# Kernel tuning notes

Hardware: AMD Instinct MI355X
Metric: run time of the kernel (lower is better)

Reference implementation:

```python
import jax, jax.numpy as jnp
import numpy as np

B, M, D, E, K = 4096, 4, 1024, 8, 2
H = 4 * D  # expert hidden dim (input_dim * 4)


def setup_inputs() -> dict:
    key = jax.random.key(0)
    k0, k1, k2, k3 = jax.random.split(key, 4)
    x = jax.random.normal(k0, (B, M, D), jnp.float32)
    Wg = jax.random.normal(k1, (D, E), jnp.float32) * (D ** -0.5)
    bg = jnp.zeros((E,), jnp.float32)
    W1 = jax.random.normal(k2, (E, D, H), jnp.float32) * (D ** -0.5)
    b1 = jnp.zeros((E, H), jnp.float32)
    W2 = jax.random.normal(k3, (E, H, D), jnp.float32) * (H ** -0.5)
    b2 = jnp.zeros((E, D), jnp.float32)
    return {"x": x, "Wg": Wg, "bg": bg, "W1": W1, "b1": b1, "W2": W2, "b2": b2}


def reference(x, Wg, bg, W1, b1, W2, b2):
    Bn, Mn, Dn = x.shape
    xf = x.reshape(-1, Dn)                      # [N, D], N = B*M
    logits = xf @ Wg + bg                       # [N, E] gating scores (eval: no noise)
    topv, topi = jax.lax.top_k(logits, K)       # [N, K]
    topw = jax.nn.softmax(topv, axis=-1)        # softmax over top-k only
    # scatter top-k weights into dense [N, E] gate matrix (zeros elsewhere)
    gates = jnp.sum(jax.nn.one_hot(topi, E, dtype=xf.dtype) * topw[..., None], axis=1)

    def body(acc, p):
        W1e, b1e, W2e, b2e, ge = p
        # Expert MLP: Linear -> exact GELU (torch nn.GELU default) -> Linear
        y = jax.nn.gelu(xf @ W1e + b1e, approximate=False) @ W2e + b2e
        return acc + ge[:, None] * y, None

    out, _ = jax.lax.scan(body, jnp.zeros_like(xf), (W1, b1, W2, b2, gates.T))
    return out.reshape(Bn, Mn, Dn)
```

## Files before the change

kernel.cpp:

```cpp
#include <hip/hip_runtime.h>
#include <hip/hip_bf16.h>
#include <cstdint>
#include <cstddef>

#define NTOK 16384
#define DIM 1024
#define NEXP 8
#define HDIM 4096
#define BM 256
#define BN 256
#define BK 64
#define MAXTILES 160
#define GRIDX_COMB 160
#define GRIDX_FALL 80
#define GEMM_SMEM 131072

typedef unsigned short u16;
typedef short bf16x8 __attribute__((ext_vector_type(8)));
typedef float f32x4 __attribute__((ext_vector_type(4)));

typedef const __attribute__((address_space(1))) void* gas_ptr;
typedef __attribute__((address_space(3))) void* las_ptr;

__device__ __forceinline__ void gload16(const void* g, void* l) {
  __builtin_amdgcn_global_load_lds((gas_ptr)g, (las_ptr)l, 16, 0, 0);
}

__device__ __forceinline__ u16 f2b(float f) {
  union { float f; unsigned u; } v;
  v.f = f;
  unsigned r = v.u + 0x7fffu + ((v.u >> 16) & 1u);
  return (u16)(r >> 16);
}

__device__ __forceinline__ int2 swz_block() {
  int GX = gridDim.x;
  int nwg = GX * (int)gridDim.y;
  int bid = (int)blockIdx.y * GX + (int)blockIdx.x;
  int q = nwg >> 3, r = nwg & 7;
  int xcd = bid & 7, idx = bid >> 3;
  int wg = (xcd < r) ? (xcd * (q + 1) + idx)
                     : (r * (q + 1) + (xcd - r) * q + idx);
  return make_int2(wg % GX, wg / GX);
}

__global__ __launch_bounds__(256) void gating_kernel(
    const float* __restrict__ x, const float* __restrict__ Wg,
    const float* __restrict__ bg, int* __restrict__ e01,
    float2* __restrict__ w01, int* __restrict__ counts, u16* __restrict__ xb)
{
  __shared__ float4 wgl[NEXP][256];
  __shared__ int lcnt[16];
  int t = threadIdx.x;
  if (t < 16) lcnt[t] = 0;
  float* wglf = (float*)wgl;
  const float4* wg4 = (const float4*)Wg;
  for (int i = t; i < 2048; i += 256) {
    float4 v = wg4[i];
    int d = i >> 1, eb = (i & 1) * 4;
    wglf[(eb + 0) * 1024 + d] = v.x;
    wglf[(eb + 1) * 1024 + d] = v.y;
    wglf[(eb + 2) * 1024 + d] = v.z;
    wglf[(eb + 3) * 1024 + d] = v.w;
  }
  __syncthreads();
  int lane = t & 63, wid = t >> 6;
  int tok0 = blockIdx.x * 16 + wid * 4;
  for (int s = 0; s < 4; ++s) {
    int n = tok0 + s;
    const float4* xr = (const float4*)(x + (size_t)n * DIM);
    float4 xv[4];
    #pragma unroll
    for (int k = 0; k < 4; ++k) xv[k] = xr[lane + k * 64];
    ushort4* xo = (ushort4*)(xb + (size_t)n * DIM);
    #pragma unroll
    for (int k = 0; k < 4; ++k) {
      ushort4 o;
      o.x = f2b(xv[k].x); o.y = f2b(xv[k].y); o.z = f2b(xv[k].z); o.w = f2b(xv[k].w);
      xo[lane + k * 64] = o;
    }
    double acc[NEXP];
    #pragma unroll
    for (int e = 0; e < NEXP; ++e) acc[e] = 0.0;
    #pragma unroll
    for (int k = 0; k < 4; ++k) {
      #pragma unroll
      for (int e = 0; e < NEXP; ++e) {
        float4 w = wgl[e][lane + k * 64];
        acc[e] += (double)(xv[k].x * w.x) + (double)(xv[k].y * w.y)
                + (double)(xv[k].z * w.z) + (double)(xv[k].w * w.w);
      }
    }
    #pragma unroll
    for (int e = 0; e < NEXP; ++e) {
      for (int off = 32; off; off >>= 1) acc[e] += __shfl_down(acc[e], off, 64);
    }
    if (lane == 0) {
      float v[NEXP];
      #pragma unroll
      for (int e = 0; e < NEXP; ++e) v[e] = (float)acc[e] + bg[e];
      int e0 = 0; float v0 = v[0];
      #pragma unroll
      for (int e = 1; e < NEXP; ++e) if (v[e] > v0) { v0 = v[e]; e0 = e; }
      int e1 = -1; float v1 = -1e30f;
      #pragma unroll
      for (int e = 0; e < NEXP; ++e) if (e != e0 && v[e] > v1) { v1 = v[e]; e1 = e; }
      float d = expf(v1 - v0);
      float w0 = 1.0f / (1.0f + d);
      float w1 = d * w0;
      e01[n] = e0 | (e1 << 8);
      w01[n] = make_float2(w0, w1);
      atomicAdd(&lcnt[e0], 1);
      atomicAdd(&lcnt[8 + e1], 1);
    }
  }
  __syncthreads();
  if (t < 16 && lcnt[t]) atomicAdd(&counts[t], lcnt[t]);
}

__global__ void plan_kernel(const int* __restrict__ counts, int* __restrict__ offsets,
                            int* __restrict__ cursors, int* __restrict__ numTiles,
                            int4* __restrict__ tiledir, int combined)
{
  if (threadIdx.x == 0 && blockIdx.x == 0) {
    for (int p = 0; p < 2; ++p) {
      int o = 0;
      for (int e = 0; e < NEXP; ++e) {
        offsets[p * 8 + e] = o;
        cursors[p * 8 + e] = o;
        o += counts[p * 8 + e];
      }
    }
    if (combined) {
      int idx = 0;
      for (int s = 0; s < 16; ++s) {
        int p = s >> 3, e = s & 7;
        int c = counts[s];
        int base = p * NTOK + offsets[s];
        for (int st = 0; st < c; st += BM) {
          tiledir[idx] = make_int4(e, base + st, (c - st) < BM ? (c - st) : BM, 0);
          ++idx;
        }
      }
      numTiles[0] = idx;
      numTiles[1] = 0;
    } else {
      for (int p = 0; p < 2; ++p) {
        int idx = 0;
        for (int e = 0; e < NEXP; ++e) {
          int c = counts[p * 8 + e];
          int base = p * NTOK + offsets[p * 8 + e];
          for (int st = 0; st < c; st += BM) {
            tiledir[p * MAXTILES + idx] = make_int4(e, base + st, (c - st) < BM ? (c - st) : BM, 0);
            ++idx;
          }
        }
        numTiles[p] = idx;
      }
    }
  }
}

__global__ __launch_bounds__(256) void scatter_kernel(
    const int* __restrict__ e01, const float2* __restrict__ w01,
    int* __restrict__ cursors, int* __restrict__ rowlist, float* __restrict__ roww)
{
  int n = blockIdx.x * 256 + threadIdx.x;
  int ee = e01[n];
  float2 w = w01[n];
  int e0 = ee & 255, e1 = ee >> 8;
  int p0 = atomicAdd(&cursors[e0], 1);
  rowlist[p0] = n; roww[p0] = w.x;
  int p1 = atomicAdd(&cursors[8 + e1], 1);
  rowlist[NTOK + p1] = n; roww[NTOK + p1] = w.y;
}

__global__ __launch_bounds__(256) void transpose_convert_kernel(
    const float* __restrict__ in, u16* __restrict__ out, int R, int C)
{
  __shared__ float tile[64][65];
  size_t base = (size_t)blockIdx.z * R * C;
  int r0 = blockIdx.x * 64, c0 = blockIdx.y * 64;
  int t = threadIdx.x;
  int lr = t >> 4, lc4 = (t & 15) * 4;
  #pragma unroll
  for (int i = 0; i < 4; ++i) {
    float4 v = *reinterpret_cast<const float4*>(
        &in[base + (size_t)(r0 + i * 16 + lr) * C + c0 + lc4]);
    tile[i * 16 + lr][lc4 + 0] = v.x;
    tile[i * 16 + lr][lc4 + 1] = v.y;
    tile[i * 16 + lr][lc4 + 2] = v.z;
    tile[i * 16 + lr][lc4 + 3] = v.w;
  }
  __syncthreads();
  #pragma unroll
  for (int i = 0; i < 4; ++i) {
    int oc = i * 16 + lr;
    ushort4 o;
    o.x = f2b(tile[lc4 + 0][oc]);
    o.y = f2b(tile[lc4 + 1][oc]);
    o.z = f2b(tile[lc4 + 2][oc]);
    o.w = f2b(tile[lc4 + 3][oc]);
    *reinterpret_cast<ushort4*>(&out[base + (size_t)(c0 + oc) * R + r0 + lc4]) = o;
  }
}


__global__ __launch_bounds__(512, 2) void gemm1_kernel(
    const u16* __restrict__ xb, const u16* __restrict__ w1t,
    const float* __restrict__ b1, u16* __restrict__ h,
    const int* __restrict__ rowlist, const int4* __restrict__ tiledir,
    const int* __restrict__ numTiles, int hbase)
{
  extern __shared__ u16 smem[];
  u16* Aldsb = smem;
  u16* Bldsb = smem + 32768;
  __shared__ int tok[BM];
  int2 bxy = swz_block();
  int bx = bxy.x, by = bxy.y;
  if (bx >= *numTiles) return;
  int4 td = tiledir[bx];
  int e = td.x, row0 = td.y, rows = td.z;
  int n0 = by * BN;
  int t = threadIdx.x, lane = t & 63, wid = t >> 6;
  for (int i = t; i < BM; i += 512) {
    int p = row0 + i; if (p > 2 * NTOK - 1) p = 2 * NTOK - 1;
    tok[i] = rowlist[p];
  }
  __syncthreads();
  int schunk = (lane & 7) ^ (lane >> 3);
  const u16* gA[4]; const u16* gB[4];
  #pragma unroll
  for (int i = 0; i < 4; ++i) {
    int row = (wid * 4 + i) * 8 + (lane >> 3);
    gA[i] = xb + (size_t)tok[row] * DIM + schunk * 8;
    gB[i] = w1t + ((size_t)e * HDIM + n0 + row) * DIM + schunk * 8;
  }
  f32x4 acc[8][4] = {};
  int wr = wid >> 2, wc = wid & 3;
  int arow = lane & 15, cbase = lane >> 4, csw = arow & 7;
  #pragma unroll
  for (int i = 0; i < 4; ++i) {
    gload16(gA[i], &Aldsb[(wid * 4 + i) * 512]);
    gload16(gB[i], &Bldsb[(wid * 4 + i) * 512]);
  }
  __syncthreads();
  const int NKT = DIM / BK;
  for (int kt = 0; kt < NKT; ++kt) {
    int buf = kt & 1;
    if (kt + 1 < NKT) {
      int bo = (buf ^ 1) * 16384;
      #pragma unroll
      for (int i = 0; i < 4; ++i) {
        gload16(gA[i] + (kt + 1) * BK, &Aldsb[bo + (wid * 4 + i) * 512]);
        gload16(gB[i] + (kt + 1) * BK, &Bldsb[bo + (wid * 4 + i) * 512]);
      }
    }
    const u16* Ab = Aldsb + buf * 16384;
    const u16* Bb = Bldsb + buf * 16384;
    #pragma unroll
    for (int kk = 0; kk < 2; ++kk) {
      int cp = ((kk * 4 + cbase) ^ csw) * 8;
      bf16x8 a[8], b[4];
      #pragma unroll
      for (int m = 0; m < 8; ++m)
        a[m] = *reinterpret_cast<const bf16x8*>(&Ab[(wr * 128 + m * 16 + arow) * BK + cp]);
      #pragma unroll
      for (int n = 0; n < 4; ++n)
        b[n] = *reinterpret_cast<const bf16x8*>(&Bb[(wc * 64 + n * 16 + arow) * BK + cp]);
      __builtin_amdgcn_s_setprio(1);
      #pragma unroll
      for (int m = 0; m < 8; ++m)
        #pragma unroll
        for (int n = 0; n < 4; ++n)
          acc[m][n] = __builtin_amdgcn_mfma_f32_16x16x32_bf16(a[m], b[n], acc[m][n], 0, 0, 0);
      __builtin_amdgcn_s_setprio(0);
    }
    __syncthreads();
  }
  int rsub = (lane >> 4) * 4;
  #pragma unroll
  for (int m = 0; m < 8; ++m) {
    int lrb = wr * 128 + m * 16 + rsub;
    #pragma unroll
    for (int n = 0; n < 4; ++n) {
      int col = n0 + wc * 64 + n * 16 + arow;
      float bv = b1[e * HDIM + col];
      #pragma unroll
      for (int r = 0; r < 4; ++r) {
        int lr = lrb + r;
        if (lr < rows) {
          float v = acc[m][n][r] + bv;
          v = 0.5f * v * (1.0f + erff(v * 0.70710678118654752f));
          h[(size_t)(row0 + lr - hbase) * HDIM + col] = f2b(v);
        }
      }
    }
  }
}

__global__ __launch_bounds__(512, 2) void gemm2_kernel(
    const u16* __restrict__ h, const u16* __restrict__ w2t,
    const float* __restrict__ b2, float* __restrict__ out,
    const int* __restrict__ rowlist, const float* __restrict__ roww,
    const int4* __restrict__ tiledir, const int* __restrict__ numTiles, int hbase)
{
  extern __shared__ u16 smem[];
  u16* Aldsb = smem;
  u16* Bldsb = smem + 32768;
  __shared__ int tok[BM];
  __shared__ float wt[BM];
  int2 bxy = swz_block();
  int bx = bxy.x, by = bxy.y;
  if (bx >= *numTiles) return;
  int4 td = tiledir[bx];
  int e = td.x, row0 = td.y, rows = td.z;
  int n0 = by * BN;
  int t = threadIdx.x, lane = t & 63, wid = t >> 6;
  for (int i = t; i < BM; i += 512) {
    int p = row0 + i; if (p > 2 * NTOK - 1) p = 2 * NTOK - 1;
    tok[i] = rowlist[p];
    wt[i] = roww[p];
  }
  int schunk = (lane & 7) ^ (lane >> 3);
  const u16* gA[4]; const u16* gB[4];
  #pragma unroll
  for (int i = 0; i < 4; ++i) {
    int row = (wid * 4 + i) * 8 + (lane >> 3);
    int hr = row < rows ? row : (rows - 1);
    gA[i] = h + (size_t)(row0 + hr - hbase) * HDIM + schunk * 8;
    gB[i] = w2t + ((size_t)e * DIM + n0 + row) * HDIM + schunk * 8;
  }
  f32x4 acc[8][4] = {};
  int wr = wid >> 2, wc = wid & 3;
  int arow = lane & 15, cbase = lane >> 4, csw = arow & 7;
  #pragma unroll
  for (int i = 0; i < 4; ++i) {
    gload16(gA[i], &Aldsb[(wid * 4 + i) * 512]);
    gload16(gB[i], &Bldsb[(wid * 4 + i) * 512]);
  }
  __syncthreads();
  const int NKT = HDIM / BK;
  for (int kt = 0; kt < NKT; ++kt) {
    int buf = kt & 1;
    if (kt + 1 < NKT) {
      int bo = (buf ^ 1) * 16384;
      #pragma unroll
      for (int i = 0; i < 4; ++i) {
        gload16(gA[i] + (kt + 1) * BK, &Aldsb[bo + (wid * 4 + i) * 512]);
        gload16(gB[i] + (kt + 1) * BK, &Bldsb[bo + (wid * 4 + i) * 512]);
      }
    }
    const u16* Ab = Aldsb + buf * 16384;
    const u16* Bb = Bldsb + buf * 16384;
    #pragma unroll
    for (int kk = 0; kk < 2; ++kk) {
      int cp = ((kk * 4 + cbase) ^ csw) * 8;
      bf16x8 a[8], b[4];
      #pragma unroll
      for (int m = 0; m < 8; ++m)
        a[m] = *reinterpret_cast<const bf16x8*>(&Ab[(wr * 128 + m * 16 + arow) * BK + cp]);
      #pragma unroll
      for (int n = 0; n < 4; ++n)
        b[n] = *reinterpret_cast<const bf16x8*>(&Bb[(wc * 64 + n * 16 + arow) * BK + cp]);
      __builtin_amdgcn_s_setprio(1);
      #pragma unroll
      for (int m = 0; m < 8; ++m)
        #pragma unroll
        for (int n = 0; n < 4; ++n)
          acc[m][n] = __builtin_amdgcn_mfma_f32_16x16x32_bf16(a[m], b[n], acc[m][n], 0, 0, 0);
      __builtin_amdgcn_s_setprio(0);
    }
    __syncthreads();
  }
  int rsub = (lane >> 4) * 4;
  #pragma unroll
  for (int m = 0; m < 8; ++m) {
    int lrb = wr * 128 + m * 16 + rsub;
    #pragma unroll
    for (int n = 0; n < 4; ++n) {
      int col = n0 + wc * 64 + n * 16 + arow;
      float bv = b2[e * DIM + col];
      #pragma unroll
      for (int r = 0; r < 4; ++r) {
        int lr = lrb + r;
        if (lr < rows) {
          float v = (acc[m][n][r] + bv) * wt[lr];
          atomicAdd(&out[(size_t)tok[lr] * DIM + col], v);
        }
      }
    }
  }
}

extern "C" void kernel_launch(void* const* d_in, const int* in_sizes, int n_in,
                              void* d_out, int out_size, void* d_ws, size_t ws_size,
                              hipStream_t stream)
{
  const float* x  = (const float*)d_in[0];
  const float* Wg = (const float*)d_in[1];
  const float* bg = (const float*)d_in[2];
  const float* W1 = (const float*)d_in[3];
  const float* b1 = (const float*)d_in[4];
  const float* W2 = (const float*)d_in[5];
  const float* b2 = (const float*)d_in[6];
  float* out = (float*)d_out;

  const size_t SZ_XB  = (size_t)NTOK * DIM * 2;
  const size_t SZ_W1T = (size_t)NEXP * DIM * HDIM * 2;
  const size_t SZ_W2T = (size_t)NEXP * HDIM * DIM * 2;
  const size_t SZ_H1  = (size_t)NTOK * HDIM * 2;
  const size_t SZ_TAIL = (size_t)2 * NTOK * 4 + (size_t)2 * NTOK * 4
                       + (size_t)NTOK * 4 + (size_t)NTOK * 8 + 256
                       + (size_t)2 * MAXTILES * 16 + 1024;
  const size_t NEED_COMB = SZ_XB + SZ_W1T + SZ_W2T + 2 * SZ_H1 + SZ_TAIL;
  int combined = (ws_size >= NEED_COMB) ? 1 : 0;
  size_t szh = combined ? 2 * SZ_H1 : SZ_H1;

  char* ws = (char*)d_ws;
  const size_t OFF_XB  = 0;
  const size_t OFF_W1T = OFF_XB  + SZ_XB;
  const size_t OFF_W2T = OFF_W1T + SZ_W1T;
  const size_t OFF_H   = OFF_W2T + SZ_W2T;
  const size_t OFF_RL  = OFF_H   + szh;
  const size_t OFF_RW  = OFF_RL  + (size_t)2 * NTOK * 4;
  const size_t OFF_E01 = OFF_RW  + (size_t)2 * NTOK * 4;
  const size_t OFF_W01 = OFF_E01 + (size_t)NTOK * 4;
  const size_t OFF_META= OFF_W01 + (size_t)NTOK * 8;
  const size_t OFF_DIR = OFF_META + 256;

  u16*    xb      = (u16*)(ws + OFF_XB);
  u16*    w1t     = (u16*)(ws + OFF_W1T);
  u16*    w2t     = (u16*)(ws + OFF_W2T);
  u16*    h       = (u16*)(ws + OFF_H);
  int*    rowlist = (int*)(ws + OFF_RL);
  float*  roww    = (float*)(ws + OFF_RW);
  int*    e01     = (int*)(ws + OFF_E01);
  float2* w01     = (float2*)(ws + OFF_W01);
  int*    meta    = (int*)(ws + OFF_META);
  int*    counts   = meta;
  int*    offsets  = meta + 16;
  int*    cursors  = meta + 32;
  int*    numTiles = meta + 48;
  int4*   tiledir  = (int4*)(ws + OFF_DIR);

  hipMemsetAsync(meta, 0, 256, stream);
  hipMemsetAsync(out, 0, (size_t)out_size * 4, stream);

  gating_kernel<<<NTOK / 16, 256, 0, stream>>>(x, Wg, bg, e01, w01, counts, xb);
  plan_kernel<<<1, 64, 0, stream>>>(counts, offsets, cursors, numTiles, tiledir, combined);
  scatter_kernel<<<NTOK / 256, 256, 0, stream>>>(e01, w01, cursors, rowlist, roww);

  transpose_convert_kernel<<<dim3(DIM / 64, HDIM / 64, NEXP), 256, 0, stream>>>(W1, w1t, DIM, HDIM);
  transpose_convert_kernel<<<dim3(HDIM / 64, DIM / 64, NEXP), 256, 0, stream>>>(W2, w2t, HDIM, DIM);

  if (combined) {
    gemm1_kernel<<<dim3(GRIDX_COMB, HDIM / BN), 512, GEMM_SMEM, stream>>>(
        xb, w1t, b1, h, rowlist, tiledir, numTiles, 0);
    gemm2_kernel<<<dim3(GRIDX_COMB, DIM / BN), 512, GEMM_SMEM, stream>>>(
        h, w2t, b2, out, rowlist, roww, tiledir, numTiles, 0);
  } else {
    gemm1_kernel<<<dim3(GRIDX_FALL, HDIM / BN), 512, GEMM_SMEM, stream>>>(
        xb, w1t, b1, h, rowlist, tiledir, numTiles, 0);
    gemm2_kernel<<<dim3(GRIDX_FALL, DIM / BN), 512, GEMM_SMEM, stream>>>(
        h, w2t, b2, out, rowlist, roww, tiledir, numTiles, 0);
    gemm1_kernel<<<dim3(GRIDX_FALL, HDIM / BN), 512, GEMM_SMEM, stream>>>(
        xb, w1t, b1, h, rowlist, tiledir + MAXTILES, numTiles + 1, NTOK);
    gemm2_kernel<<<dim3(GRIDX_FALL, DIM / BN), 512, GEMM_SMEM, stream>>>(
        h, w2t, b2, out, rowlist, roww, tiledir + MAXTILES, numTiles + 1, NTOK);
  }
}
```

Before: 1.236 ms.

## Halve GEMM K-tile to 32 with a pair-row swizzled LDS layout

Reduces the K tile of both expert GEMMs from 64 to 32, halving the LDS footprint (128KB to 64KB). A new swizzled LDS layout packs two rows per 64-element line so each direct-to-LDS load and bf16x8 fragment read stays conflict-free. The intent is lower LDS pressure and possibly more resident blocks per CU. The trade-off is twice as many K iterations and barriers, with fewer MFMAs between each sync.

```diff
diff --git a/kernel.cpp b/kernel.cpp
--- a/kernel.cpp
+++ b/kernel.cpp
@@ -9,11 +9,11 @@
 #define HDIM 4096
 #define BM 256
 #define BN 256
-#define BK 64
+#define BK 32
 #define MAXTILES 160
 #define GRIDX_COMB 160
 #define GRIDX_FALL 80
-#define GEMM_SMEM 131072
+#define GEMM_SMEM 65536
 
 typedef unsigned short u16;
 typedef short bf16x8 __attribute__((ext_vector_type(8)));
@@ -214,7 +214,7 @@
 {
   extern __shared__ u16 smem[];
   u16* Aldsb = smem;
-  u16* Bldsb = smem + 32768;
+  u16* Bldsb = smem + 16384;
   __shared__ int tok[BM];
   int2 bxy = swz_block();
   int bx = bxy.x, by = bxy.y;
@@ -228,54 +228,57 @@
     tok[i] = rowlist[p];
   }
   __syncthreads();
-  int schunk = (lane & 7) ^ (lane >> 3);
-  const u16* gA[4]; const u16* gB[4];
-  #pragma unroll
-  for (int i = 0; i < 4; ++i) {
-    int row = (wid * 4 + i) * 8 + (lane >> 3);
-    gA[i] = xb + (size_t)tok[row] * DIM + schunk * 8;
-    gB[i] = w1t + ((size_t)e * HDIM + n0 + row) * DIM + schunk * 8;
+  int qoff[2]; const u16* gA[2]; const u16* gB[2];
+  #pragma unroll
+  for (int j = 0; j < 2; ++j) {
+    int q = wid * 128 + j * 64 + lane;
+    int p = q >> 3, pos8 = q & 7;
+    int pl = pos8 ^ (p & 7);
+    int row = p * 2 + (pl >> 2);
+    int c = pl & 3;
+    qoff[j] = q * 8;
+    gA[j] = xb + (size_t)tok[row] * DIM + c * 8;
+    gB[j] = w1t + ((size_t)e * HDIM + n0 + row) * DIM + c * 8;
   }
   f32x4 acc[8][4] = {};
   int wr = wid >> 2, wc = wid & 3;
-  int arow = lane & 15, cbase = lane >> 4, csw = arow & 7;
-  #pragma unroll
-  for (int i = 0; i < 4; ++i) {
-    gload16(gA[i], &Aldsb[(wid * 4 + i) * 512]);
-    gload16(gB[i], &Bldsb[(wid * 4 + i) * 512]);
+  int arow = lane & 15, cbase = lane >> 4;
+  int pos8r = (((arow & 1) << 2) | cbase) ^ ((arow >> 1) & 7);
+  int aBase = wr * 4096 + (arow >> 1) * 64 + pos8r * 8;
+  int bBase = wc * 2048 + (arow >> 1) * 64 + pos8r * 8;
+  #pragma unroll
+  for (int j = 0; j < 2; ++j) {
+    gload16(gA[j], &Aldsb[qoff[j]]);
+    gload16(gB[j], &Bldsb[qoff[j]]);
   }
   __syncthreads();
   const int NKT = DIM / BK;
   for (int kt = 0; kt < NKT; ++kt) {
     int buf = kt & 1;
     if (kt + 1 < NKT) {
-      int bo = (buf ^ 1) * 16384;
-      #pragma unroll
-      for (int i = 0; i < 4; ++i) {
-        gload16(gA[i] + (kt + 1) * BK, &Aldsb[bo + (wid * 4 + i) * 512]);
-        gload16(gB[i] + (kt + 1) * BK, &Bldsb[bo + (wid * 4 + i) * 512]);
-      }
-    }
-    const u16* Ab = Aldsb + buf * 16384;
-    const u16* Bb = Bldsb + buf * 16384;
-    #pragma unroll
-    for (int kk = 0; kk < 2; ++kk) {
-      int cp = ((kk * 4 + cbase) ^ csw) * 8;
-      bf16x8 a[8], b[4];
-      #pragma unroll
-      for (int m = 0; m < 8; ++m)
-        a[m] = *reinterpret_cast<const bf16x8*>(&Ab[(wr * 128 + m * 16 + arow) * BK + cp]);
+      int bo = (buf ^ 1) * 8192;
+      #pragma unroll
+      for (int j = 0; j < 2; ++j) {
+        gload16(gA[j] + (kt + 1) * BK, &Aldsb[bo + qoff[j]]);
+        gload16(gB[j] + (kt + 1) * BK, &Bldsb[bo + qoff[j]]);
+      }
+    }
+    const u16* Ab = Aldsb + buf * 8192;
+    const u16* Bb = Bldsb + buf * 8192;
+    bf16x8 a[8], b[4];
+    #pragma unroll
+    for (int m = 0; m < 8; ++m)
+      a[m] = *reinterpret_cast<const bf16x8*>(&Ab[aBase + m * 512]);
+    #pragma unroll
+    for (int n = 0; n < 4; ++n)
+      b[n] = *reinterpret_cast<const bf16x8*>(&Bb[bBase + n * 512]);
+    __builtin_amdgcn_s_setprio(1);
+    #pragma unroll
+    for (int m = 0; m < 8; ++m)
       #pragma unroll
       for (int n = 0; n < 4; ++n)
-        b[n] = *reinterpret_cast<const bf16x8*>(&Bb[(wc * 64 + n * 16 + arow) * BK + cp]);
-      __builtin_amdgcn_s_setprio(1);
-      #pragma unroll
-      for (int m = 0; m < 8; ++m)
-        #pragma unroll
-        for (int n = 0; n < 4; ++n)
-          acc[m][n] = __builtin_amdgcn_mfma_f32_16x16x32_bf16(a[m], b[n], acc[m][n], 0, 0, 0);
-      __builtin_amdgcn_s_setprio(0);
-    }
+        acc[m][n] = __builtin_amdgcn_mfma_f32_16x16x32_bf16(a[m], b[n], acc[m][n], 0, 0, 0);
+    __builtin_amdgcn_s_setprio(0);
     __syncthreads();
   }
   int rsub = (lane >> 4) * 4;
@@ -307,7 +310,7 @@
 {
   extern __shared__ u16 smem[];
   u16* Aldsb = smem;
-  u16* Bldsb = smem + 32768;
+  u16* Bldsb = smem + 16384;
   __shared__ int tok[BM];
   __shared__ float wt[BM];
   int2 bxy = swz_block();
@@ -322,55 +325,58 @@
     tok[i] = rowlist[p];
     wt[i] = roww[p];
   }
-  int schunk = (lane & 7) ^ (lane >> 3);
-  const u16* gA[4]; const u16* gB[4];
-  #pragma unroll
-  for (int i = 0; i < 4; ++i) {
-    int row = (wid * 4 + i) * 8 + (lane >> 3);
+  int qoff[2]; const u16* gA[2]; const u16* gB[2];
+  #pragma unroll
+  for (int j = 0; j < 2; ++j) {
+    int q = wid * 128 + j * 64 + lane;
+    int p = q >> 3, pos8 = q & 7;
+    int pl = pos8 ^ (p & 7);
+    int row = p * 2 + (pl >> 2);
+    int c = pl & 3;
+    qoff[j] = q * 8;
     int hr = row < rows ? row : (rows - 1);
-    gA[i] = h + (size_t)(row0 + hr - hbase) * HDIM + schunk * 8;
-    gB[i] = w2t + ((size_t)e * DIM + n0 + row) * HDIM + schunk * 8;
+    gA[j] = h + (size_t)(row0 + hr - hbase) * HDIM + c * 8;
+    gB[j] = w2t + ((size_t)e * DIM + n0 + row) * HDIM + c * 8;
   }
   f32x4 acc[8][4] = {};
   int wr = wid >> 2, wc = wid & 3;
-  int arow = lane & 15, cbase = lane >> 4, csw = arow & 7;
-  #pragma unroll
-  for (int i = 0; i < 4; ++i) {
-    gload16(gA[i], &Aldsb[(wid * 4 + i) * 512]);
-    gload16(gB[i], &Bldsb[(wid * 4 + i) * 512]);
+  int arow = lane & 15, cbase = lane >> 4;
+  int pos8r = (((arow & 1) << 2) | cbase) ^ ((arow >> 1) & 7);
+  int aBase = wr * 4096 + (arow >> 1) * 64 + pos8r * 8;
+  int bBase = wc * 2048 + (arow >> 1) * 64 + pos8r * 8;
+  #pragma unroll
+  for (int j = 0; j < 2; ++j) {
+    gload16(gA[j], &Aldsb[qoff[j]]);
+    gload16(gB[j], &Bldsb[qoff[j]]);
   }
   __syncthreads();
   const int NKT = HDIM / BK;
   for (int kt = 0; kt < NKT; ++kt) {
     int buf = kt & 1;
     if (kt + 1 < NKT) {
-      int bo = (buf ^ 1) * 16384;
-      #pragma unroll
-      for (int i = 0; i < 4; ++i) {
-        gload16(gA[i] + (kt + 1) * BK, &Aldsb[bo + (wid * 4 + i) * 512]);
-        gload16(gB[i] + (kt + 1) * BK, &Bldsb[bo + (wid * 4 + i) * 512]);
-      }
-    }
-    const u16* Ab = Aldsb + buf * 16384;
-    const u16* Bb = Bldsb + buf * 16384;
-    #pragma unroll
-    for (int kk = 0; kk < 2; ++kk) {
-      int cp = ((kk * 4 + cbase) ^ csw) * 8;
-      bf16x8 a[8], b[4];
-      #pragma unroll
-      for (int m = 0; m < 8; ++m)
-        a[m] = *reinterpret_cast<const bf16x8*>(&Ab[(wr * 128 + m * 16 + arow) * BK + cp]);
+      int bo = (buf ^ 1) * 8192;
+      #pragma unroll
+      for (int j = 0; j < 2; ++j) {
+        gload16(gA[j] + (kt + 1) * BK, &Aldsb[bo + qoff[j]]);
+        gload16(gB[j] + (kt + 1) * BK, &Bldsb[bo + qoff[j]]);
+      }
+    }
+    const u16* Ab = Aldsb + buf * 8192;
+    const u16* Bb = Bldsb + buf * 8192;
+    bf16x8 a[8], b[4];
+    #pragma unroll
+    for (int m = 0; m < 8; ++m)
+      a[m] = *reinterpret_cast<const bf16x8*>(&Ab[aBase + m * 512]);
+    #pragma unroll
+    for (int n = 0; n < 4; ++n)
+      b[n] = *reinterpret_cast<const bf16x8*>(&Bb[bBase + n * 512]);
+    __builtin_amdgcn_s_setprio(1);
+    #pragma unroll
+    for (int m = 0; m < 8; ++m)
       #pragma unroll
       for (int n = 0; n < 4; ++n)
-        b[n] = *reinterpret_cast<const bf16x8*>(&Bb[(wc * 64 + n * 16 + arow) * BK + cp]);
-      __builtin_amdgcn_s_setprio(1);
-      #pragma unroll
-      for (int m = 0; m < 8; ++m)
-        #pragma unroll
-        for (int n = 0; n < 4; ++n)
-          acc[m][n] = __builtin_amdgcn_mfma_f32_16x16x32_bf16(a[m], b[n], acc[m][n], 0, 0, 0);
-      __builtin_amdgcn_s_setprio(0);
-    }
+        acc[m][n] = __builtin_amdgcn_mfma_f32_16x16x32_bf16(a[m], b[n], acc[m][n], 0, 0, 0);
+    __builtin_amdgcn_s_setprio(0);
     __syncthreads();
   }
   int rsub = (lane >> 4) * 4;
```

New measurement: 1.370 ms. +10.9%, slower.
